# Performance work log

Measured on AMD Instinct MI355X. Metric: run time of the kernel, lower is better.

## Reference

```python
import jax, jax.numpy as jnp
import numpy as np

NUM_CLUSTERS = 64
DIM = 512
ALPHA = 100.0
EPS = 1e-12  # torch F.normalize eps


def setup_inputs() -> dict:
    key = jax.random.key(0)
    k1, k2 = jax.random.split(key)
    x1 = jax.random.normal(k1, (30, DIM, 28, 28), dtype=jnp.float32)
    centroids = jax.random.uniform(k2, (NUM_CLUSTERS, DIM), dtype=jnp.float32)
    # _init_params: conv weight = 2*alpha*centroids (1x1 conv), bias = -alpha*||centroid||
    conv_w = 2.0 * ALPHA * centroids
    conv_b = -ALPHA * jnp.linalg.norm(centroids, axis=1)
    return {"x1": x1, "centroids": centroids, "conv_w": conv_w, "conv_b": conv_b}


def _l2norm(v, axis):
    n = jnp.sqrt(jnp.sum(v * v, axis=axis, keepdims=True))
    return v / jnp.maximum(n, EPS)


def reference(x1, centroids, conv_w, conv_b):
    T, C, H, W = x1.shape
    K, D = centroids.shape
    x = x1.reshape(T, C, H * W)            # [T, C, N]
    x = _l2norm(x, axis=1)                 # normalize_input: L2 over channel dim
    # 1x1 conv == matmul over channels: logits [T, K, N]
    logits = jnp.einsum('kc,tcn->tkn', conv_w, x) + conv_b[None, :, None]
    a = jax.nn.softmax(logits, axis=1)     # soft assignment over clusters
    # vlad[t,k,c] = sum_n a[t,k,n]*(x[t,c,n] - centroids[k,c])
    # rewritten as two small matmuls, avoiding the [K,C,N] residual tensor
    vlad = jnp.einsum('tkn,tcn->tkc', a, x) - a.sum(axis=-1)[:, :, None] * centroids[None]
    vlad = _l2norm(vlad, axis=2)           # intra-normalization over feature dim
    v = vlad.reshape(T, K * D)
    v = _l2norm(v, axis=1)                 # global L2 normalization
    return v.sum(axis=0, keepdims=True)    # [1, K*D] accumulated over 30 timesteps
```

## Files before the change

### kernel.cpp

```cpp
#include <hip/hip_runtime.h>
#include <math.h>

#define T_ 30
#define C_ 512
#define N_ 784
#define NA_ 832
#define PITCH 129
#define EPSV 1e-12f

typedef __attribute__((ext_vector_type(8))) short bf16x8;
typedef __attribute__((ext_vector_type(4))) float f32x4;
typedef __attribute__((ext_vector_type(4))) int i32x4;

__device__ __forceinline__ unsigned short f2bf(float f) {
    union { float f; unsigned int u; } v; v.f = f;
    unsigned int r = (v.u + 0x7FFFu + ((v.u >> 16) & 1u)) >> 16;
    return (unsigned short)r;
}
__device__ __forceinline__ float bf2f(unsigned short h) {
    union { unsigned int u; float f; } v; v.u = ((unsigned int)h) << 16;
    return v.f;
}

__global__ void k_prep(const float* __restrict__ w, unsigned short* __restrict__ wh,
                       unsigned short* __restrict__ wl) {
    int idx = blockIdx.x * 256 + threadIdx.x;
    float v = w[idx];
    unsigned short h = f2bf(v);
    wh[idx] = h;
    wl[idx] = f2bf(v - bf2f(h));
}

__global__ __launch_bounds__(256) void k_assign(
    const float* __restrict__ x, const unsigned short* __restrict__ wh,
    const unsigned short* __restrict__ wl, const float* __restrict__ b,
    unsigned short* __restrict__ aT, float* __restrict__ asum)
{
    __shared__ unsigned int xpk[64 * PITCH];
    __shared__ float ssq[64];
    int t = blockIdx.y, n0 = blockIdx.x * 64;
    int tid = threadIdx.x;
    int w = tid >> 6, L = tid & 63, lid = L & 15, quad = L >> 4;
    int nseg = (tid & 15) * 4;
    int crow = tid >> 4;

    if (tid < 64) ssq[tid] = 0.f;
    float ss[4] = {0.f, 0.f, 0.f, 0.f};

    f32x4 acc[4];
    #pragma unroll
    for (int mt = 0; mt < 4; ++mt)
        #pragma unroll
        for (int r = 0; r < 4; ++r) acc[mt][r] = 0.f;

    for (int cc = 0; cc < 4; ++cc) {
        #pragma unroll
        for (int p = 0; p < 8; ++p) {
            int cl = p * 16 + crow;
            int c = cc * 128 + cl;
            int n = n0 + nseg;
            float4 q = make_float4(0.f, 0.f, 0.f, 0.f);
            if (n < N_)
                q = *reinterpret_cast<const float4*>(x + ((size_t)t * C_ + c) * N_ + n);
            float vv[4] = {q.x, q.y, q.z, q.w};
            #pragma unroll
            for (int j = 0; j < 4; ++j) {
                float v = vv[j];
                ss[j] = fmaf(v, v, ss[j]);
                union { float f; unsigned int u; } cv; cv.f = v;
                unsigned int hiw = cv.u & 0xFFFF0000u;
                union { unsigned int u; float f; } hv; hv.u = hiw;
                unsigned int lo = f2bf(v - hv.f);
                xpk[(nseg + j) * PITCH + cl] = hiw | lo;
            }
        }
        if (cc == 3) {
            #pragma unroll
            for (int j = 0; j < 4; ++j) {
                ss[j] += __shfl_xor(ss[j], 16, 64);
                ss[j] += __shfl_xor(ss[j], 32, 64);
            }
            if ((tid & 48) == 0) {
                #pragma unroll
                for (int j = 0; j < 4; ++j) atomicAdd(&ssq[nseg + j], ss[j]);
            }
        }
        __syncthreads();
        #pragma unroll
        for (int ks = 0; ks < 4; ++ks) {
            int cl0 = ks * 32 + quad * 8;
            unsigned int u[8];
            #pragma unroll
            for (int e = 0; e < 8; ++e)
                u[e] = xpk[(w * 16 + lid) * PITCH + cl0 + e];
            union { i32x4 v; bf16x8 b; } bh, bl;
            #pragma unroll
            for (int e2 = 0; e2 < 4; ++e2) {
                bh.v[e2] = (int)((u[2 * e2] >> 16) | (u[2 * e2 + 1] & 0xFFFF0000u));
                bl.v[e2] = (int)((u[2 * e2] & 0xFFFFu) | (u[2 * e2 + 1] << 16));
            }
            int cs = cc * 128 + ks * 32 + quad * 8;
            #pragma unroll
            for (int mt = 0; mt < 4; ++mt) {
                bf16x8 ah = *reinterpret_cast<const bf16x8*>(wh + (size_t)(mt * 16 + lid) * C_ + cs);
                bf16x8 al = *reinterpret_cast<const bf16x8*>(wl + (size_t)(mt * 16 + lid) * C_ + cs);
                acc[mt] = __builtin_amdgcn_mfma_f32_16x16x32_bf16(ah, bh.b, acc[mt], 0, 0, 0);
                acc[mt] = __builtin_amdgcn_mfma_f32_16x16x32_bf16(al, bh.b, acc[mt], 0, 0, 0);
                acc[mt] = __builtin_amdgcn_mfma_f32_16x16x32_bf16(ah, bl.b, acc[mt], 0, 0, 0);
            }
        }
        __syncthreads();
    }

    int n_lane = n0 + w * 16 + lid;
    bool valid = n_lane < N_;
    float inv = 0.f;
    if (valid) inv = 1.0f / fmaxf(sqrtf(ssq[w * 16 + lid]), EPSV);

    float lg[16];
    float mx = -1e30f;
    #pragma unroll
    for (int mt = 0; mt < 4; ++mt) {
        f32x4 bv = *reinterpret_cast<const f32x4*>(b + mt * 16 + quad * 4);
        #pragma unroll
        for (int r = 0; r < 4; ++r) {
            float v = fmaf(acc[mt][r], inv, bv[r]);
            lg[mt * 4 + r] = v;
            mx = fmaxf(mx, v);
        }
    }
    mx = fmaxf(mx, __shfl_xor(mx, 16, 64));
    mx = fmaxf(mx, __shfl_xor(mx, 32, 64));
    float se = 0.f;
    #pragma unroll
    for (int u = 0; u < 16; ++u) { lg[u] = __expf(lg[u] - mx); se += lg[u]; }
    se += __shfl_xor(se, 16, 64);
    se += __shfl_xor(se, 32, 64);
    float rs = 1.0f / se;

    size_t abase = (size_t)t * 64 * NA_ + n_lane;
    #pragma unroll
    for (int mt = 0; mt < 4; ++mt)
        #pragma unroll
        for (int r = 0; r < 4; ++r) {
            int k = mt * 16 + quad * 4 + r;
            float a = lg[mt * 4 + r] * rs;
            aT[abase + (size_t)k * NA_] = valid ? f2bf(a * inv) : (unsigned short)0;
            float ak = valid ? a : 0.f;
            ak += __shfl_xor(ak, 1, 64); ak += __shfl_xor(ak, 2, 64);
            ak += __shfl_xor(ak, 4, 64); ak += __shfl_xor(ak, 8, 64);
            if (lid == 0) atomicAdd(&asum[t * 64 + k], ak);
        }
}

__global__ __launch_bounds__(256) void k_vlad(
    const float* __restrict__ x, const unsigned short* __restrict__ aT,
    const float* __restrict__ asum, const float* __restrict__ cent,
    float* __restrict__ vlad, float* __restrict__ g2)
{
    __shared__ float red[4][16 * 68];
    int t = blockIdx.y, c0 = blockIdx.x * 16;
    int tid = threadIdx.x;
    int w = tid >> 6, L = tid & 63, lid = L & 15, quad = L >> 4;

    f32x4 acc[4];
    #pragma unroll
    for (int mt = 0; mt < 4; ++mt)
        #pragma unroll
        for (int r = 0; r < 4; ++r) acc[mt][r] = 0.f;

    const float* xrow = x + ((size_t)t * C_ + c0 + lid) * N_;
    const unsigned short* ab = aT + (size_t)t * 64 * NA_;

    for (int s = w; s < 26; s += 4) {
        int nb = s * 32 + quad * 8;
        int nbc = nb > 776 ? 776 : nb;
        float4 x0 = *reinterpret_cast<const float4*>(xrow + nbc);
        float4 x1 = *reinterpret_cast<const float4*>(xrow + nbc + 4);
        bf16x8 bb;
        bb[0] = (short)f2bf(x0.x); bb[1] = (short)f2bf(x0.y);
        bb[2] = (short)f2bf(x0.z); bb[3] = (short)f2bf(x0.w);
        bb[4] = (short)f2bf(x1.x); bb[5] = (short)f2bf(x1.y);
        bb[6] = (short)f2bf(x1.z); bb[7] = (short)f2bf(x1.w);
        #pragma unroll
        for (int mt = 0; mt < 4; ++mt) {
            bf16x8 af = *reinterpret_cast<const bf16x8*>(ab + (size_t)(mt * 16 + lid) * NA_ + nb);
            acc[mt] = __builtin_amdgcn_mfma_f32_16x16x32_bf16(af, bb, acc[mt], 0, 0, 0);
        }
    }
    {
        float* rp = &red[w][0];
        #pragma unroll
        for (int mt = 0; mt < 4; ++mt)
            *reinterpret_cast<f32x4*>(&rp[lid * 68 + mt * 16 + quad * 4]) = acc[mt];
    }
    __syncthreads();

    int k = tid >> 2, cs4 = (tid & 3) * 4;
    float as = asum[t * 64 + k];
    float4 cv = *reinterpret_cast<const float4*>(cent + k * C_ + c0 + cs4);
    float4 vout;
    float s2 = 0.f;
    #pragma unroll
    for (int j = 0; j < 4; ++j) {
        int cc = cs4 + j;
        float v = red[0][cc * 68 + k] + red[1][cc * 68 + k]
                + red[2][cc * 68 + k] + red[3][cc * 68 + k];
        v -= as * ((const float*)&cv)[j];
        ((float*)&vout)[j] = v;
        s2 = fmaf(v, v, s2);
    }
    *reinterpret_cast<float4*>(vlad + ((size_t)t * 64 + k) * C_ + c0 + cs4) = vout;
    s2 += __shfl_xor(s2, 1, 64);
    s2 += __shfl_xor(s2, 2, 64);
    if ((tid & 3) == 0) atomicAdd(&g2[t * 64 + k], s2);
}

__global__ __launch_bounds__(256) void k_out(
    const float* __restrict__ vlad, const float* __restrict__ g2,
    float* __restrict__ out)
{
    __shared__ float intr[1920];
    __shared__ float sinv[T_];
    int tid = threadIdx.x;
    for (int i = tid; i < 1920; i += 256)
        intr[i] = 1.0f / fmaxf(sqrtf(g2[i]), EPSV);
    __syncthreads();
    if (tid < T_) {
        float s = 0.f;
        #pragma unroll 8
        for (int k = 0; k < 64; ++k) {
            float iv = intr[tid * 64 + k];
            s += g2[tid * 64 + k] * iv * iv;
        }
        sinv[tid] = 1.0f / fmaxf(sqrtf(s), EPSV);
    }
    __syncthreads();
    int idx = blockIdx.x * 256 + tid;
    int k = idx >> 9;
    float s = 0.f;
    #pragma unroll 5
    for (int t = 0; t < T_; ++t)
        s += vlad[(size_t)t * 32768 + idx] * intr[t * 64 + k] * sinv[t];
    out[idx] = s;
}

extern "C" void kernel_launch(void* const* d_in, const int* in_sizes, int n_in,
                              void* d_out, int out_size, void* d_ws, size_t ws_size,
                              hipStream_t stream) {
    const float* x    = (const float*)d_in[0];
    const float* cent = (const float*)d_in[1];
    const float* w    = (const float*)d_in[2];
    const float* b    = (const float*)d_in[3];
    float* out = (float*)d_out;

    char* p = (char*)d_ws;
    unsigned short* wh = (unsigned short*)p;  p += 65536;
    unsigned short* wl = (unsigned short*)p;  p += 65536;
    float* asum = (float*)p;                  p += 1920 * 4;
    float* g2   = (float*)p;                  p += 1920 * 4;
    unsigned short* aT = (unsigned short*)p;  p += (size_t)T_ * 64 * NA_ * 2;
    float* vlad = (float*)p;                  p += (size_t)T_ * 64 * C_ * 4;

    k_prep<<<128, 256, 0, stream>>>(w, wh, wl);
    hipMemsetAsync(asum, 0, 2 * 1920 * 4, stream);
    k_assign<<<dim3(13, T_), 256, 0, stream>>>(x, wh, wl, b, aT, asum);
    k_vlad<<<dim3(32, T_), 256, 0, stream>>>(x, aT, asum, cent, vlad, g2);
    k_out<<<128, 256, 0, stream>>>(vlad, g2, out);
}
```

Before: 155.2 us.

## Split assignment kernel into channel-split logits GEMM and separate softmax kernel

The fused assign kernel is split in two. A logits kernel runs over 2 channel halves per tile, which doubles the grid from 390 to 780 blocks, and writes partial logits plus atomically accumulated sum-of-squares to workspace. A new softmax kernel sums the two partials, normalizes, computes the softmax, and writes the transposed bf16 assignments and per-cluster sums through shared memory. This trades extra global traffic (about 13 MB of partial logits) and one more launch for better GPU occupancy in the GEMM phase.

```diff
diff --git a/kernel.cpp b/kernel.cpp
--- a/kernel.cpp
+++ b/kernel.cpp
@@ -4,8 +4,8 @@
 #define T_ 30
 #define C_ 512
 #define N_ 784
+#define NW_ 832
 #define NA_ 832
-#define PITCH 129
 #define EPSV 1e-12f
 
 typedef __attribute__((ext_vector_type(8))) short bf16x8;
@@ -31,20 +31,23 @@
     wl[idx] = f2bf(v - bf2f(h));
 }
 
-__global__ __launch_bounds__(256) void k_assign(
+__global__ __launch_bounds__(256) void k_logits(
     const float* __restrict__ x, const unsigned short* __restrict__ wh,
-    const unsigned short* __restrict__ wl, const float* __restrict__ b,
-    unsigned short* __restrict__ aT, float* __restrict__ asum)
+    const unsigned short* __restrict__ wl, float* __restrict__ logitsH,
+    float* __restrict__ logitsL, float* __restrict__ sumsq)
 {
-    __shared__ unsigned int xpk[64 * PITCH];
-    __shared__ float ssq[64];
-    int t = blockIdx.y, n0 = blockIdx.x * 64;
+    __shared__ __align__(16) char smem[64 * 129 * 4];
+    unsigned int* stage = (unsigned int*)smem;
+    float* red = (float*)smem;
+
+    int nt = blockIdx.x, ch = blockIdx.y, t = blockIdx.z;
+    int n0 = nt * 64;
     int tid = threadIdx.x;
     int w = tid >> 6, L = tid & 63, lid = L & 15, quad = L >> 4;
+
+    int clb = tid >> 4;
     int nseg = (tid & 15) * 4;
-    int crow = tid >> 4;
-
-    if (tid < 64) ssq[tid] = 0.f;
+    bool vld = (n0 + nseg) < N_;
     float ss[4] = {0.f, 0.f, 0.f, 0.f};
 
     f32x4 acc[4];
@@ -53,36 +56,26 @@
         #pragma unroll
         for (int r = 0; r < 4; ++r) acc[mt][r] = 0.f;
 
-    for (int cc = 0; cc < 4; ++cc) {
+    #pragma unroll
+    for (int cc = 0; cc < 2; ++cc) {
+        int cbase = ch * 256 + cc * 128;
         #pragma unroll
         for (int p = 0; p < 8; ++p) {
-            int cl = p * 16 + crow;
-            int c = cc * 128 + cl;
-            int n = n0 + nseg;
+            int cl = p * 16 + clb;
             float4 q = make_float4(0.f, 0.f, 0.f, 0.f);
-            if (n < N_)
-                q = *reinterpret_cast<const float4*>(x + ((size_t)t * C_ + c) * N_ + n);
+            if (vld)
+                q = *reinterpret_cast<const float4*>(
+                    x + ((size_t)(t * C_ + cbase + cl)) * N_ + n0 + nseg);
             float vv[4] = {q.x, q.y, q.z, q.w};
             #pragma unroll
             for (int j = 0; j < 4; ++j) {
                 float v = vv[j];
                 ss[j] = fmaf(v, v, ss[j]);
-                union { float f; unsigned int u; } cv; cv.f = v;
-                unsigned int hiw = cv.u & 0xFFFF0000u;
+                union { float f; unsigned int u; } cvt; cvt.f = v;
+                unsigned int hiw = cvt.u & 0xFFFF0000u;
                 union { unsigned int u; float f; } hv; hv.u = hiw;
                 unsigned int lo = f2bf(v - hv.f);
-                xpk[(nseg + j) * PITCH + cl] = hiw | lo;
-            }
-        }
-        if (cc == 3) {
-            #pragma unroll
-            for (int j = 0; j < 4; ++j) {
-                ss[j] += __shfl_xor(ss[j], 16, 64);
-                ss[j] += __shfl_xor(ss[j], 32, 64);
-            }
-            if ((tid & 48) == 0) {
-                #pragma unroll
-                for (int j = 0; j < 4; ++j) atomicAdd(&ssq[nseg + j], ss[j]);
+                stage[(nseg + j) * 129 + cl] = hiw | lo;
             }
         }
         __syncthreads();
@@ -92,14 +85,14 @@
             unsigned int u[8];
             #pragma unroll
             for (int e = 0; e < 8; ++e)
-                u[e] = xpk[(w * 16 + lid) * PITCH + cl0 + e];
+                u[e] = stage[(w * 16 + lid) * 129 + cl0 + e];
             union { i32x4 v; bf16x8 b; } bh, bl;
             #pragma unroll
             for (int e2 = 0; e2 < 4; ++e2) {
                 bh.v[e2] = (int)((u[2 * e2] >> 16) | (u[2 * e2 + 1] & 0xFFFF0000u));
                 bl.v[e2] = (int)((u[2 * e2] & 0xFFFFu) | (u[2 * e2 + 1] << 16));
             }
-            int cs = cc * 128 + ks * 32 + quad * 8;
+            int cs = cbase + ks * 32 + quad * 8;
             #pragma unroll
             for (int mt = 0; mt < 4; ++mt) {
                 bf16x8 ah = *reinterpret_cast<const bf16x8*>(wh + (size_t)(mt * 16 + lid) * C_ + cs);
@@ -112,45 +105,95 @@
         __syncthreads();
     }
 
-    int n_lane = n0 + w * 16 + lid;
-    bool valid = n_lane < N_;
-    float inv = 0.f;
-    if (valid) inv = 1.0f / fmaxf(sqrtf(ssq[w * 16 + lid]), EPSV);
+    #pragma unroll
+    for (int j = 0; j < 4; ++j) {
+        ss[j] += __shfl_xor(ss[j], 16, 64);
+        ss[j] += __shfl_xor(ss[j], 32, 64);
+    }
+    if (L < 16 && vld) {
+        #pragma unroll
+        for (int j = 0; j < 4; ++j)
+            atomicAdd(&sumsq[t * N_ + n0 + L * 4 + j], ss[j]);
+    }
+
+    {
+        float* rp = red + (w * 16 + lid) * 68;
+        #pragma unroll
+        for (int mt = 0; mt < 4; ++mt)
+            *reinterpret_cast<f32x4*>(&rp[mt * 16 + quad * 4]) = acc[mt];
+    }
+    __syncthreads();
+
+    float* dst = (ch == 0 ? logitsH : logitsL);
+    int n = tid >> 2, kseg = (tid & 3) * 16;
+    size_t base = ((size_t)t * NW_ + n0 + n) * 64 + kseg;
+    #pragma unroll
+    for (int i = 0; i < 4; ++i)
+        *reinterpret_cast<f32x4*>(dst + base + i * 4) =
+            *reinterpret_cast<f32x4*>(&red[n * 68 + kseg + i * 4]);
+}
+
+__global__ __launch_bounds__(256) void k_softmax(
+    const float* __restrict__ logitsH, const float* __restrict__ logitsL,
+    const float* __restrict__ sumsq, const float* __restrict__ b,
+    unsigned short* __restrict__ aT, float* __restrict__ asum)
+{
+    __shared__ unsigned short sT[64 * 66];
+    __shared__ float asl[64];
+    int nt = blockIdx.x, t = blockIdx.y;
+    int n0 = nt * 64;
+    int tid = threadIdx.x;
+    if (tid < 64) asl[tid] = 0.f;
+    __syncthreads();
+
+    int n = tid >> 2, kseg = (tid & 3) * 16;
+    int n_g = n0 + n;
+    bool valid = n_g < N_;
+    size_t base = ((size_t)t * NW_ + n_g) * 64 + kseg;
 
     float lg[16];
+    #pragma unroll
+    for (int i = 0; i < 4; ++i) {
+        f32x4 h = *reinterpret_cast<const f32x4*>(logitsH + base + i * 4);
+        f32x4 l = *reinterpret_cast<const f32x4*>(logitsL + base + i * 4);
+        #pragma unroll
+        for (int r = 0; r < 4; ++r) lg[i * 4 + r] = h[r] + l[r];
+    }
+    float s = valid ? sumsq[t * N_ + n_g] : 0.f;
+    float inv = 1.0f / fmaxf(sqrtf(s), EPSV);
     float mx = -1e30f;
     #pragma unroll
-    for (int mt = 0; mt < 4; ++mt) {
-        f32x4 bv = *reinterpret_cast<const f32x4*>(b + mt * 16 + quad * 4);
-        #pragma unroll
-        for (int r = 0; r < 4; ++r) {
-            float v = fmaf(acc[mt][r], inv, bv[r]);
-            lg[mt * 4 + r] = v;
-            mx = fmaxf(mx, v);
-        }
-    }
-    mx = fmaxf(mx, __shfl_xor(mx, 16, 64));
-    mx = fmaxf(mx, __shfl_xor(mx, 32, 64));
+    for (int u = 0; u < 16; ++u) {
+        lg[u] = fmaf(lg[u], inv, b[kseg + u]);
+        mx = fmaxf(mx, lg[u]);
+    }
+    mx = fmaxf(mx, __shfl_xor(mx, 1, 64));
+    mx = fmaxf(mx, __shfl_xor(mx, 2, 64));
     float se = 0.f;
     #pragma unroll
     for (int u = 0; u < 16; ++u) { lg[u] = __expf(lg[u] - mx); se += lg[u]; }
-    se += __shfl_xor(se, 16, 64);
-    se += __shfl_xor(se, 32, 64);
+    se += __shfl_xor(se, 1, 64);
+    se += __shfl_xor(se, 2, 64);
     float rs = 1.0f / se;
 
-    size_t abase = (size_t)t * 64 * NA_ + n_lane;
-    #pragma unroll
-    for (int mt = 0; mt < 4; ++mt)
-        #pragma unroll
-        for (int r = 0; r < 4; ++r) {
-            int k = mt * 16 + quad * 4 + r;
-            float a = lg[mt * 4 + r] * rs;
-            aT[abase + (size_t)k * NA_] = valid ? f2bf(a * inv) : (unsigned short)0;
-            float ak = valid ? a : 0.f;
-            ak += __shfl_xor(ak, 1, 64); ak += __shfl_xor(ak, 2, 64);
-            ak += __shfl_xor(ak, 4, 64); ak += __shfl_xor(ak, 8, 64);
-            if (lid == 0) atomicAdd(&asum[t * 64 + k], ak);
-        }
+    #pragma unroll
+    for (int u = 0; u < 16; ++u) {
+        float a = valid ? lg[u] * rs : 0.f;
+        sT[(kseg + u) * 66 + n] = valid ? f2bf(a * inv) : (unsigned short)0;
+        atomicAdd(&asl[kseg + u], a);
+    }
+    __syncthreads();
+
+    #pragma unroll
+    for (int i = 0; i < 4; ++i) {
+        int idx = tid + i * 256;
+        int k = idx >> 4, seg = (idx & 15) * 4;
+        ushort4 v4;
+        v4.x = sT[k * 66 + seg + 0]; v4.y = sT[k * 66 + seg + 1];
+        v4.z = sT[k * 66 + seg + 2]; v4.w = sT[k * 66 + seg + 3];
+        *reinterpret_cast<ushort4*>(aT + ((size_t)t * 64 + k) * NA_ + n0 + seg) = v4;
+    }
+    if (tid < 64) atomicAdd(&asum[t * 64 + tid], asl[tid]);
 }
 
 __global__ __launch_bounds__(256) void k_vlad(
@@ -257,14 +300,18 @@
     char* p = (char*)d_ws;
     unsigned short* wh = (unsigned short*)p;  p += 65536;
     unsigned short* wl = (unsigned short*)p;  p += 65536;
-    float* asum = (float*)p;                  p += 1920 * 4;
-    float* g2   = (float*)p;                  p += 1920 * 4;
+    float* sumsq = (float*)p;                 p += 30 * 784 * 4;
+    float* asum  = (float*)p;                 p += 1920 * 4;
+    float* g2    = (float*)p;                 p += 1920 * 4;
     unsigned short* aT = (unsigned short*)p;  p += (size_t)T_ * 64 * NA_ * 2;
+    float* logitsH = (float*)p;               p += (size_t)T_ * NW_ * 64 * 4;
+    float* logitsL = (float*)p;               p += (size_t)T_ * NW_ * 64 * 4;
     float* vlad = (float*)p;                  p += (size_t)T_ * 64 * C_ * 4;
 
     k_prep<<<128, 256, 0, stream>>>(w, wh, wl);
-    hipMemsetAsync(asum, 0, 2 * 1920 * 4, stream);
-    k_assign<<<dim3(13, T_), 256, 0, stream>>>(x, wh, wl, b, aT, asum);
+    hipMemsetAsync(sumsq, 0, (30 * 784 + 2 * 1920) * 4, stream);
+    k_logits<<<dim3(13, 2, T_), 256, 0, stream>>>(x, wh, wl, logitsH, logitsL, sumsq);
+    k_softmax<<<dim3(13, T_), 256, 0, stream>>>(logitsH, logitsL, sumsq, b, aT, asum);
     k_vlad<<<dim3(32, T_), 256, 0, stream>>>(x, aT, asum, cent, vlad, g2);
     k_out<<<128, 256, 0, stream>>>(vlad, g2, out);
 }
```

After: 159.3 us. 1.03x slower.
